# Kernel tuning notes

Measured on AMD Instinct MI355X. Metric: run time of the kernel, lower is better.

## Reference

```python
import jax, jax.numpy as jnp
import numpy as np

E = 16        # num_experts
H = 1024      # hidden_size
I = 768       # moe_intermediate_size
TOP_K = 2     # num_experts_per_tok
B, S = 1, 2048


def setup_inputs() -> dict:
    key = jax.random.key(0)
    ks = jax.random.split(key, 5)
    scale = 0.02
    return {
        "hidden_states": jax.random.normal(ks[0], (B, S, H), dtype=jnp.float32),
        "gate_w": jax.random.normal(ks[1], (E, H), dtype=jnp.float32) * scale,
        "gate_proj": jax.random.normal(ks[2], (E, I, H), dtype=jnp.float32) * scale,
        "up_proj": jax.random.normal(ks[3], (E, I, H), dtype=jnp.float32) * scale,
        "down_proj": jax.random.normal(ks[4], (E, H, I), dtype=jnp.float32) * scale,
    }


def reference(hidden_states, gate_w, gate_proj, up_proj, down_proj):
    b, s, h = hidden_states.shape
    x = hidden_states.reshape(-1, h)                        # [T, H]
    T = x.shape[0]

    # Router: logits -> fp32 softmax -> top-k -> renormalize (norm_topk_prob=True)
    router_logits = x @ gate_w.T                            # [T, E]
    probs = jax.nn.softmax(router_logits.astype(jnp.float32), axis=-1)
    top_vals, top_idx = jax.lax.top_k(probs, TOP_K)         # [T, k]
    top_vals = top_vals / jnp.sum(top_vals, axis=-1, keepdims=True)

    # Dense combine-weight matrix [T, E] (zero for unrouted experts)
    rw = jnp.zeros((T, E), dtype=jnp.float32)
    rw = rw.at[jnp.arange(T)[:, None], top_idx].add(top_vals)
    rw = rw.astype(hidden_states.dtype)

    # Expert SwiGLU MLPs (dense-over-experts reference for the grouped GEMM)
    g = jnp.einsum("th,eih->eti", x, gate_proj)             # [E, T, I]
    u = jnp.einsum("th,eih->eti", x, up_proj)               # [E, T, I]
    hmid = jax.nn.silu(g) * u                                # [E, T, I]
    expert_out = jnp.einsum("eti,ehi->eth", hmid, down_proj)  # [E, T, H]

    # Weighted combine
    out = jnp.einsum("eth,te->th", expert_out, rw)          # [T, H]
    return out.reshape(b, s, h)
```

## Files before the change

### kernel.cpp

```cpp
#include <hip/hip_runtime.h>
#include <hip/hip_bf16.h>
#include <cmath>

constexpr int T = 2048;
constexpr int H = 1024;
constexpr int I = 768;
constexpr int E = 16;
constexpr int WMAX = 48;

typedef short short8 __attribute__((ext_vector_type(8)));
typedef float f32x4  __attribute__((ext_vector_type(4)));

__device__ __forceinline__ short f2bf(float f) {
    __hip_bfloat16 h = __float2bfloat16(f);
    return *reinterpret_cast<short*>(&h);
}

__device__ __forceinline__ short8 pack8(float4 a, float4 b) {
    short8 v = {f2bf(a.x), f2bf(a.y), f2bf(a.z), f2bf(a.w),
                f2bf(b.x), f2bf(b.y), f2bf(b.z), f2bf(b.w)};
    return v;
}

__device__ __forceinline__ int sw(int r, int kg) {
    return r * 32 + (((kg + (r >> 1)) & 3) << 3);
}

__global__ __launch_bounds__(256) void cvt_x_kernel(
    const float* __restrict__ x, short* __restrict__ xb)
{
    size_t i = (size_t)blockIdx.x * 256 + threadIdx.x;
    const float4* s4 = (const float4*)x;
    float4 a = s4[2 * i], b = s4[2 * i + 1];
    *(short8*)(xb + i * 8) = pack8(a, b);
}

__global__ __launch_bounds__(256) void router_kernel(
    const float* __restrict__ x,
    const float* __restrict__ gw,
    int* __restrict__ cnt,
    int* __restrict__ entries,
    float* __restrict__ wlist)
{
    const int tid = threadIdx.x;
    const int tl = tid & 15, e = tid >> 4;
    const int t = blockIdx.x * 16 + tl;

    const float4* xr = (const float4*)(x + (size_t)t * H);
    const float4* gr = (const float4*)(gw + (size_t)e * H);
    float s0 = 0.f, s1 = 0.f;
    #pragma unroll 8
    for (int q = 0; q < 256; q += 2) {
        float4 a = xr[q],     b = gr[q];
        float4 c = xr[q + 1], d = gr[q + 1];
        s0 += a.x * b.x + a.y * b.y + a.z * b.z + a.w * b.w;
        s1 += c.x * d.x + c.y * d.y + c.z * d.z + c.w * d.w;
    }

    __shared__ float lg[16][17];
    lg[tl][e] = s0 + s1;
    __syncthreads();

    if (tid < 16) {
        int tk = blockIdx.x * 16 + tid;
        float v1 = -3.0e38f, v2 = -3.0e38f;
        int i1 = 0, i2 = 0;
        #pragma unroll
        for (int k = 0; k < E; ++k) {
            float v = lg[tid][k];
            if (v > v1) { v2 = v1; i2 = i1; v1 = v; i1 = k; }
            else if (v > v2) { v2 = v; i2 = k; }
        }
        float w1 = 1.f / (1.f + expf(v2 - v1));
        float w2 = 1.f - w1;
        int p = atomicAdd(&cnt[i1], 1);
        entries[i1 * T + p] = tk * 2;
        wlist[i1 * T + p] = w1;
        p = atomicAdd(&cnt[i2], 1);
        entries[i2 * T + p] = tk * 2 + 1;
        wlist[i2 * T + p] = w2;
    }
}

__global__ void build_worklist(const int* __restrict__ cnt,
                               int2* __restrict__ items,
                               int* __restrict__ nitems)
{
    if (threadIdx.x == 0) {
        int c = 0;
        for (int e = 0; e < E; ++e) {
            int n = cnt[e];
            for (int t0 = 0; t0 < n; t0 += 128) items[c++] = make_int2(e, t0);
        }
        *nitems = c;
    }
}

__global__ __launch_bounds__(256) void gateup_mfma(
    const short* __restrict__ xb,
    const float* __restrict__ gate_p,
    const float* __restrict__ up_p,
    const int* __restrict__ cnt,
    const int* __restrict__ entries,
    const int* __restrict__ nitems,
    const int2* __restrict__ items,
    short* __restrict__ hmid)
{
    if (blockIdx.x >= *nitems) return;
    const int e  = items[blockIdx.x].x;
    const int t0 = items[blockIdx.x].y;
    const int n  = cnt[e];
    const int i0 = blockIdx.y * 64;

    __shared__ short Xs[128 * 32];
    __shared__ short Gs[64 * 32];
    __shared__ short Us[64 * 32];
    __shared__ int toks[128];

    const int tid = threadIdx.x;
    if (tid < 128) {
        int r = t0 + tid;
        toks[tid] = (r < n) ? entries[e * T + r] : -1;
    }
    __syncthreads();

    const int lane = tid & 63, wave = tid >> 6;
    const int m16 = lane & 15, q = lane >> 4;

    const int sr = tid >> 2, skg = tid & 3;
    const int xt0 = toks[sr], xt1 = toks[64 + sr];
    const short* xsrc0 = xb + (size_t)((xt0 >= 0 ? xt0 : 0) >> 1) * H + skg * 8;
    const short* xsrc1 = xb + (size_t)((xt1 >= 0 ? xt1 : 0) >> 1) * H + skg * 8;
    const float* gsrc = gate_p + (size_t)e * I * H + (size_t)(i0 + sr) * H + skg * 8;
    const float* usrc = up_p   + (size_t)e * I * H + (size_t)(i0 + sr) * H + skg * 8;

    f32x4 accg[8], accu[8];
    #pragma unroll
    for (int a = 0; a < 8; ++a) {
        accg[a] = (f32x4){0.f, 0.f, 0.f, 0.f};
        accu[a] = (f32x4){0.f, 0.f, 0.f, 0.f};
    }

    short8 xc0 = *(const short8*)xsrc0;
    short8 xc1 = *(const short8*)xsrc1;
    float4 gc0 = *(const float4*)gsrc, gc1 = *(const float4*)(gsrc + 4);
    float4 uc0 = *(const float4*)usrc, uc1 = *(const float4*)(usrc + 4);

    for (int k0 = 0; k0 < H; k0 += 32) {
        *(short8*)&Xs[sw(sr, skg)]      = xc0;
        *(short8*)&Xs[sw(64 + sr, skg)] = xc1;
        *(short8*)&Gs[sw(sr, skg)] = pack8(gc0, gc1);
        *(short8*)&Us[sw(sr, skg)] = pack8(uc0, uc1);
        int kn = (k0 + 32 < H) ? k0 + 32 : 0;
        xc0 = *(const short8*)(xsrc0 + kn);
        xc1 = *(const short8*)(xsrc1 + kn);
        gc0 = *(const float4*)(gsrc + kn); gc1 = *(const float4*)(gsrc + kn + 4);
        uc0 = *(const float4*)(usrc + kn); uc1 = *(const float4*)(usrc + kn + 4);
        __syncthreads();

        short8 bg = *(const short8*)&Gs[sw(wave * 16 + m16, q)];
        short8 bu = *(const short8*)&Us[sw(wave * 16 + m16, q)];
        #pragma unroll
        for (int mi = 0; mi < 8; ++mi) {
            short8 af = *(const short8*)&Xs[sw(mi * 16 + m16, q)];
            accg[mi] = __builtin_amdgcn_mfma_f32_16x16x32_bf16(af, bg, accg[mi], 0, 0, 0);
            accu[mi] = __builtin_amdgcn_mfma_f32_16x16x32_bf16(af, bu, accu[mi], 0, 0, 0);
        }
        __syncthreads();
    }

    const int col = i0 + wave * 16 + m16;
    #pragma unroll
    for (int mi = 0; mi < 8; ++mi)
        #pragma unroll
        for (int j = 0; j < 4; ++j) {
            int row = mi * 16 + q * 4 + j;
            int slot = toks[row];
            if (slot < 0) continue;
            float g = accg[mi][j];
            float u = accu[mi][j];
            float hv = g / (1.f + expf(-g)) * u;
            ((unsigned short*)hmid)[(size_t)slot * I + col] = (unsigned short)f2bf(hv);
        }
}

__global__ __launch_bounds__(256) void down_mfma(
    const short* __restrict__ hmid,
    const float* __restrict__ down_p,
    const int* __restrict__ cnt,
    const int* __restrict__ entries,
    const float* __restrict__ wlist,
    const int* __restrict__ nitems,
    const int2* __restrict__ items,
    float* __restrict__ out)
{
    if (blockIdx.x >= *nitems) return;
    const int e  = items[blockIdx.x].x;
    const int t0 = items[blockIdx.x].y;
    const int n  = cnt[e];
    const int h0 = blockIdx.y * 128;

    __shared__ short As[128 * 32];
    __shared__ short Bs[128 * 32];
    __shared__ int toks[128];
    __shared__ float wr[128];

    const int tid = threadIdx.x;
    if (tid < 128) {
        int r = t0 + tid;
        bool v = (r < n);
        toks[tid] = v ? entries[e * T + r] : -1;
        wr[tid]   = v ? wlist[e * T + r] : 0.f;
    }
    __syncthreads();

    const int lane = tid & 63, wave = tid >> 6;
    const int m16 = lane & 15, q = lane >> 4;

    const int sr = tid >> 2, skg = tid & 3;
    const int at0 = toks[sr], at1 = toks[64 + sr];
    const short* asrc0 = hmid + (size_t)(at0 >= 0 ? at0 : 0) * I + skg * 8;
    const short* asrc1 = hmid + (size_t)(at1 >= 0 ? at1 : 0) * I + skg * 8;
    const float* bsrc0 = down_p + (size_t)e * H * I + (size_t)(h0 + sr) * I + skg * 8;
    const float* bsrc1 = down_p + (size_t)e * H * I + (size_t)(h0 + 64 + sr) * I + skg * 8;

    f32x4 acc[8][2];
    #pragma unroll
    for (int a = 0; a < 8; ++a)
        #pragma unroll
        for (int b = 0; b < 2; ++b)
            acc[a][b] = (f32x4){0.f, 0.f, 0.f, 0.f};

    short8 ac0 = *(const short8*)asrc0;
    short8 ac1 = *(const short8*)asrc1;
    float4 bc0 = *(const float4*)bsrc0, bc1 = *(const float4*)(bsrc0 + 4);
    float4 bc2 = *(const float4*)bsrc1, bc3 = *(const float4*)(bsrc1 + 4);

    for (int k0 = 0; k0 < I; k0 += 32) {
        *(short8*)&As[sw(sr, skg)]      = ac0;
        *(short8*)&As[sw(64 + sr, skg)] = ac1;
        *(short8*)&Bs[sw(sr, skg)]      = pack8(bc0, bc1);
        *(short8*)&Bs[sw(64 + sr, skg)] = pack8(bc2, bc3);
        int kn = (k0 + 32 < I) ? k0 + 32 : 0;
        ac0 = *(const short8*)(asrc0 + kn);
        ac1 = *(const short8*)(asrc1 + kn);
        bc0 = *(const float4*)(bsrc0 + kn); bc1 = *(const float4*)(bsrc0 + kn + 4);
        bc2 = *(const float4*)(bsrc1 + kn); bc3 = *(const float4*)(bsrc1 + kn + 4);
        __syncthreads();

        short8 bf0 = *(const short8*)&Bs[sw(wave * 32 + m16, q)];
        short8 bf1 = *(const short8*)&Bs[sw(wave * 32 + 16 + m16, q)];
        #pragma unroll
        for (int mi = 0; mi < 8; ++mi) {
            short8 af = *(const short8*)&As[sw(mi * 16 + m16, q)];
            acc[mi][0] = __builtin_amdgcn_mfma_f32_16x16x32_bf16(af, bf0, acc[mi][0], 0, 0, 0);
            acc[mi][1] = __builtin_amdgcn_mfma_f32_16x16x32_bf16(af, bf1, acc[mi][1], 0, 0, 0);
        }
        __syncthreads();
    }

    #pragma unroll
    for (int mi = 0; mi < 8; ++mi)
        #pragma unroll
        for (int ni = 0; ni < 2; ++ni)
            #pragma unroll
            for (int j = 0; j < 4; ++j) {
                int row = mi * 16 + q * 4 + j;
                int slot = toks[row];
                if (slot < 0) continue;
                int t = slot >> 1;
                float w = wr[row];
                int col = h0 + wave * 32 + ni * 16 + m16;
                atomicAdd(&out[(size_t)t * H + col], w * acc[mi][ni][j]);
            }
}

extern "C" void kernel_launch(void* const* d_in, const int* in_sizes, int n_in,
                              void* d_out, int out_size, void* d_ws, size_t ws_size,
                              hipStream_t stream) {
    const float* x  = (const float*)d_in[0];
    const float* gw = (const float*)d_in[1];
    const float* gp = (const float*)d_in[2];
    const float* up = (const float*)d_in[3];
    const float* dp = (const float*)d_in[4];
    float* out = (float*)d_out;

    char* ws = (char*)d_ws;
    int*   cnt     = (int*)ws;
    int*   nitems  = (int*)(ws + 64);
    int2*  items   = (int2*)(ws + 128);
    int*   entries = (int*)(ws + 2048);
    float* wlist   = (float*)(ws + 2048 + 131072);
    short* xb      = (short*)(ws + 2048 + 262144);
    short* hmid    = xb + (size_t)T * H;

    hipMemsetAsync(ws, 0, 2048, stream);
    hipMemsetAsync(out, 0, (size_t)T * H * sizeof(float), stream);

    cvt_x_kernel<<<T * H / 2048, 256, 0, stream>>>(x, xb);
    router_kernel<<<T / 16, 256, 0, stream>>>(x, gw, cnt, entries, wlist);
    build_worklist<<<1, 64, 0, stream>>>(cnt, items, nitems);
    gateup_mfma<<<dim3(WMAX, I / 64), 256, 0, stream>>>(
        xb, gp, up, cnt, entries, nitems, items, hmid);
    down_mfma<<<dim3(WMAX, H / 128), 256, 0, stream>>>(
        hmid, dp, cnt, entries, wlist, nitems, items, out);
}
```

Measured before the change: 307.4 us.

## Fuse x conversion into router, double-buffer LDS and shrink GEMM N-tiles

Folds the fp32-to-bf16 conversion of x into the router kernel, removing a separate launch. Both expert GEMM kernels get double-buffered shared memory, so the next K-slice is stored while MFMAs run on the current one, with one barrier per iteration instead of two. N-tiles shrink (64 to 32 columns for gate/up, 128 to 64 for down), doubling the grid for more parallelism, and each wave now owns a 32-row M slice. The cost is more blocks re-reading the same gathered activation rows and less reuse per weight tile.

New measurement: 317.7 us. 3.3% more time.

```diff
diff --git a/kernel.cpp b/kernel.cpp
--- a/kernel.cpp
+++ b/kernel.cpp
@@ -26,21 +26,13 @@
     return r * 32 + (((kg + (r >> 1)) & 3) << 3);
 }
 
-__global__ __launch_bounds__(256) void cvt_x_kernel(
-    const float* __restrict__ x, short* __restrict__ xb)
-{
-    size_t i = (size_t)blockIdx.x * 256 + threadIdx.x;
-    const float4* s4 = (const float4*)x;
-    float4 a = s4[2 * i], b = s4[2 * i + 1];
-    *(short8*)(xb + i * 8) = pack8(a, b);
-}
-
 __global__ __launch_bounds__(256) void router_kernel(
     const float* __restrict__ x,
     const float* __restrict__ gw,
     int* __restrict__ cnt,
     int* __restrict__ entries,
-    float* __restrict__ wlist)
+    float* __restrict__ wlist,
+    short* __restrict__ xb)
 {
     const int tid = threadIdx.x;
     const int tl = tid & 15, e = tid >> 4;
@@ -55,6 +47,15 @@
         float4 c = xr[q + 1], d = gr[q + 1];
         s0 += a.x * b.x + a.y * b.y + a.z * b.z + a.w * b.w;
         s1 += c.x * d.x + c.y * d.y + c.z * d.z + c.w * d.w;
+    }
+
+    {
+        const int row16 = tid >> 4, c16 = tid & 15;
+        const float4* src = (const float4*)(x + (size_t)(blockIdx.x * 16 + row16) * H + c16 * 64);
+        short* dst = xb + (size_t)(blockIdx.x * 16 + row16) * H + c16 * 64;
+        #pragma unroll
+        for (int j = 0; j < 8; ++j)
+            *(short8*)(dst + j * 8) = pack8(src[2 * j], src[2 * j + 1]);
     }
 
     __shared__ float lg[16][17];
@@ -110,11 +111,11 @@
     const int e  = items[blockIdx.x].x;
     const int t0 = items[blockIdx.x].y;
     const int n  = cnt[e];
-    const int i0 = blockIdx.y * 64;
-
-    __shared__ short Xs[128 * 32];
-    __shared__ short Gs[64 * 32];
-    __shared__ short Us[64 * 32];
+    const int i0 = blockIdx.y * 32;
+
+    __shared__ short Xs[2][128 * 32];
+    __shared__ short Gs[2][32 * 32];
+    __shared__ short Us[2][32 * 32];
     __shared__ int toks[128];
 
     const int tid = threadIdx.x;
@@ -126,62 +127,84 @@
 
     const int lane = tid & 63, wave = tid >> 6;
     const int m16 = lane & 15, q = lane >> 4;
+    const int wm = wave * 32;
 
     const int sr = tid >> 2, skg = tid & 3;
     const int xt0 = toks[sr], xt1 = toks[64 + sr];
     const short* xsrc0 = xb + (size_t)((xt0 >= 0 ? xt0 : 0) >> 1) * H + skg * 8;
     const short* xsrc1 = xb + (size_t)((xt1 >= 0 ? xt1 : 0) >> 1) * H + skg * 8;
-    const float* gsrc = gate_p + (size_t)e * I * H + (size_t)(i0 + sr) * H + skg * 8;
-    const float* usrc = up_p   + (size_t)e * I * H + (size_t)(i0 + sr) * H + skg * 8;
-
-    f32x4 accg[8], accu[8];
+    const int wt = tid >> 7;
+    const int st = tid & 127, wrr = st >> 2, wkg = st & 3;
+    const float* wsrc = (wt ? up_p : gate_p)
+        + (size_t)e * I * H + (size_t)(i0 + wrr) * H + wkg * 8;
+
+    f32x4 accg[2][2], accu[2][2];
     #pragma unroll
-    for (int a = 0; a < 8; ++a) {
-        accg[a] = (f32x4){0.f, 0.f, 0.f, 0.f};
-        accu[a] = (f32x4){0.f, 0.f, 0.f, 0.f};
-    }
-
-    short8 xc0 = *(const short8*)xsrc0;
-    short8 xc1 = *(const short8*)xsrc1;
-    float4 gc0 = *(const float4*)gsrc, gc1 = *(const float4*)(gsrc + 4);
-    float4 uc0 = *(const float4*)usrc, uc1 = *(const float4*)(usrc + 4);
-
-    for (int k0 = 0; k0 < H; k0 += 32) {
-        *(short8*)&Xs[sw(sr, skg)]      = xc0;
-        *(short8*)&Xs[sw(64 + sr, skg)] = xc1;
-        *(short8*)&Gs[sw(sr, skg)] = pack8(gc0, gc1);
-        *(short8*)&Us[sw(sr, skg)] = pack8(uc0, uc1);
-        int kn = (k0 + 32 < H) ? k0 + 32 : 0;
-        xc0 = *(const short8*)(xsrc0 + kn);
-        xc1 = *(const short8*)(xsrc1 + kn);
-        gc0 = *(const float4*)(gsrc + kn); gc1 = *(const float4*)(gsrc + kn + 4);
-        uc0 = *(const float4*)(usrc + kn); uc1 = *(const float4*)(usrc + kn + 4);
+    for (int a = 0; a < 2; ++a)
+        #pragma unroll
+        for (int b = 0; b < 2; ++b) {
+            accg[a][b] = (f32x4){0.f, 0.f, 0.f, 0.f};
+            accu[a][b] = (f32x4){0.f, 0.f, 0.f, 0.f};
+        }
+
+    {
+        short8 x0 = *(const short8*)xsrc0;
+        short8 x1 = *(const short8*)xsrc1;
+        float4 wa = *(const float4*)wsrc, wb = *(const float4*)(wsrc + 4);
+        *(short8*)&Xs[0][sw(sr, skg)]      = x0;
+        *(short8*)&Xs[0][sw(64 + sr, skg)] = x1;
+        short8 pw = pack8(wa, wb);
+        if (wt == 0) *(short8*)&Gs[0][sw(wrr, wkg)] = pw;
+        else         *(short8*)&Us[0][sw(wrr, wkg)] = pw;
+    }
+    __syncthreads();
+
+    constexpr int NIT = H / 32;
+    for (int it = 0; it < NIT; ++it) {
+        const int cur = it & 1, nxt = cur ^ 1;
+        const int kn = (it + 1 < NIT) ? (it + 1) * 32 : 0;
+        short8 nx0 = *(const short8*)(xsrc0 + kn);
+        short8 nx1 = *(const short8*)(xsrc1 + kn);
+        float4 nwa = *(const float4*)(wsrc + kn), nwb = *(const float4*)(wsrc + kn + 4);
+
+        short8 af0 = *(const short8*)&Xs[cur][sw(wm + m16, q)];
+        short8 af1 = *(const short8*)&Xs[cur][sw(wm + 16 + m16, q)];
+        short8 bg0 = *(const short8*)&Gs[cur][sw(m16, q)];
+        short8 bg1 = *(const short8*)&Gs[cur][sw(16 + m16, q)];
+        short8 bu0 = *(const short8*)&Us[cur][sw(m16, q)];
+        short8 bu1 = *(const short8*)&Us[cur][sw(16 + m16, q)];
+        accg[0][0] = __builtin_amdgcn_mfma_f32_16x16x32_bf16(af0, bg0, accg[0][0], 0, 0, 0);
+        accg[1][0] = __builtin_amdgcn_mfma_f32_16x16x32_bf16(af1, bg0, accg[1][0], 0, 0, 0);
+        accg[0][1] = __builtin_amdgcn_mfma_f32_16x16x32_bf16(af0, bg1, accg[0][1], 0, 0, 0);
+        accg[1][1] = __builtin_amdgcn_mfma_f32_16x16x32_bf16(af1, bg1, accg[1][1], 0, 0, 0);
+        accu[0][0] = __builtin_amdgcn_mfma_f32_16x16x32_bf16(af0, bu0, accu[0][0], 0, 0, 0);
+        accu[1][0] = __builtin_amdgcn_mfma_f32_16x16x32_bf16(af1, bu0, accu[1][0], 0, 0, 0);
+        accu[0][1] = __builtin_amdgcn_mfma_f32_16x16x32_bf16(af0, bu1, accu[0][1], 0, 0, 0);
+        accu[1][1] = __builtin_amdgcn_mfma_f32_16x16x32_bf16(af1, bu1, accu[1][1], 0, 0, 0);
+
+        *(short8*)&Xs[nxt][sw(sr, skg)]      = nx0;
+        *(short8*)&Xs[nxt][sw(64 + sr, skg)] = nx1;
+        short8 pw = pack8(nwa, nwb);
+        if (wt == 0) *(short8*)&Gs[nxt][sw(wrr, wkg)] = pw;
+        else         *(short8*)&Us[nxt][sw(wrr, wkg)] = pw;
         __syncthreads();
-
-        short8 bg = *(const short8*)&Gs[sw(wave * 16 + m16, q)];
-        short8 bu = *(const short8*)&Us[sw(wave * 16 + m16, q)];
-        #pragma unroll
-        for (int mi = 0; mi < 8; ++mi) {
-            short8 af = *(const short8*)&Xs[sw(mi * 16 + m16, q)];
-            accg[mi] = __builtin_amdgcn_mfma_f32_16x16x32_bf16(af, bg, accg[mi], 0, 0, 0);
-            accu[mi] = __builtin_amdgcn_mfma_f32_16x16x32_bf16(af, bu, accu[mi], 0, 0, 0);
-        }
-        __syncthreads();
-    }
-
-    const int col = i0 + wave * 16 + m16;
+    }
+
     #pragma unroll
-    for (int mi = 0; mi < 8; ++mi)
-        #pragma unroll
-        for (int j = 0; j < 4; ++j) {
-            int row = mi * 16 + q * 4 + j;
-            int slot = toks[row];
-            if (slot < 0) continue;
-            float g = accg[mi][j];
-            float u = accu[mi][j];
-            float hv = g / (1.f + expf(-g)) * u;
-            ((unsigned short*)hmid)[(size_t)slot * I + col] = (unsigned short)f2bf(hv);
-        }
+    for (int mi = 0; mi < 2; ++mi)
+        #pragma unroll
+        for (int ni = 0; ni < 2; ++ni)
+            #pragma unroll
+            for (int j = 0; j < 4; ++j) {
+                int row = wm + mi * 16 + q * 4 + j;
+                int slot = toks[row];
+                if (slot < 0) continue;
+                float g = accg[mi][ni][j];
+                float u = accu[mi][ni][j];
+                float hv = g / (1.f + expf(-g)) * u;
+                int col = i0 + ni * 16 + m16;
+                ((unsigned short*)hmid)[(size_t)slot * I + col] = (unsigned short)f2bf(hv);
+            }
 }
 
 __global__ __launch_bounds__(256) void down_mfma(
@@ -198,10 +221,10 @@
     const int e  = items[blockIdx.x].x;
     const int t0 = items[blockIdx.x].y;
     const int n  = cnt[e];
-    const int h0 = blockIdx.y * 128;
-
-    __shared__ short As[128 * 32];
-    __shared__ short Bs[128 * 32];
+    const int h0 = blockIdx.y * 64;
+
+    __shared__ short As[2][128 * 32];
+    __shared__ short Bs[2][64 * 32];
     __shared__ int toks[128];
     __shared__ float wr[128];
 
@@ -216,61 +239,66 @@
 
     const int lane = tid & 63, wave = tid >> 6;
     const int m16 = lane & 15, q = lane >> 4;
+    const int wm = wave * 32;
 
     const int sr = tid >> 2, skg = tid & 3;
     const int at0 = toks[sr], at1 = toks[64 + sr];
     const short* asrc0 = hmid + (size_t)(at0 >= 0 ? at0 : 0) * I + skg * 8;
     const short* asrc1 = hmid + (size_t)(at1 >= 0 ? at1 : 0) * I + skg * 8;
-    const float* bsrc0 = down_p + (size_t)e * H * I + (size_t)(h0 + sr) * I + skg * 8;
-    const float* bsrc1 = down_p + (size_t)e * H * I + (size_t)(h0 + 64 + sr) * I + skg * 8;
-
-    f32x4 acc[8][2];
+    const float* bsrc = down_p + (size_t)e * H * I + (size_t)(h0 + sr) * I + skg * 8;
+
+    f32x4 acc[2][4];
     #pragma unroll
-    for (int a = 0; a < 8; ++a)
-        #pragma unroll
-        for (int b = 0; b < 2; ++b)
+    for (int a = 0; a < 2; ++a)
+        #pragma unroll
+        for (int b = 0; b < 4; ++b)
             acc[a][b] = (f32x4){0.f, 0.f, 0.f, 0.f};
 
-    short8 ac0 = *(const short8*)asrc0;
-    short8 ac1 = *(const short8*)asrc1;
-    float4 bc0 = *(const float4*)bsrc0, bc1 = *(const float4*)(bsrc0 + 4);
-    float4 bc2 = *(const float4*)bsrc1, bc3 = *(const float4*)(bsrc1 + 4);
-
-    for (int k0 = 0; k0 < I; k0 += 32) {
-        *(short8*)&As[sw(sr, skg)]      = ac0;
-        *(short8*)&As[sw(64 + sr, skg)] = ac1;
-        *(short8*)&Bs[sw(sr, skg)]      = pack8(bc0, bc1);
-        *(short8*)&Bs[sw(64 + sr, skg)] = pack8(bc2, bc3);
-        int kn = (k0 + 32 < I) ? k0 + 32 : 0;
-        ac0 = *(const short8*)(asrc0 + kn);
-        ac1 = *(const short8*)(asrc1 + kn);
-        bc0 = *(const float4*)(bsrc0 + kn); bc1 = *(const float4*)(bsrc0 + kn + 4);
-        bc2 = *(const float4*)(bsrc1 + kn); bc3 = *(const float4*)(bsrc1 + kn + 4);
+    {
+        short8 a0 = *(const short8*)asrc0;
+        short8 a1 = *(const short8*)asrc1;
+        float4 ba = *(const float4*)bsrc, bb = *(const float4*)(bsrc + 4);
+        *(short8*)&As[0][sw(sr, skg)]      = a0;
+        *(short8*)&As[0][sw(64 + sr, skg)] = a1;
+        *(short8*)&Bs[0][sw(sr, skg)] = pack8(ba, bb);
+    }
+    __syncthreads();
+
+    constexpr int NIT = I / 32;
+    for (int it = 0; it < NIT; ++it) {
+        const int cur = it & 1, nxt = cur ^ 1;
+        const int kn = (it + 1 < NIT) ? (it + 1) * 32 : 0;
+        short8 na0 = *(const short8*)(asrc0 + kn);
+        short8 na1 = *(const short8*)(asrc1 + kn);
+        float4 nba = *(const float4*)(bsrc + kn), nbb = *(const float4*)(bsrc + kn + 4);
+
+        short8 af0 = *(const short8*)&As[cur][sw(wm + m16, q)];
+        short8 af1 = *(const short8*)&As[cur][sw(wm + 16 + m16, q)];
+        #pragma unroll
+        for (int ni = 0; ni < 4; ++ni) {
+            short8 bfr = *(const short8*)&Bs[cur][sw(ni * 16 + m16, q)];
+            acc[0][ni] = __builtin_amdgcn_mfma_f32_16x16x32_bf16(af0, bfr, acc[0][ni], 0, 0, 0);
+            acc[1][ni] = __builtin_amdgcn_mfma_f32_16x16x32_bf16(af1, bfr, acc[1][ni], 0, 0, 0);
+        }
+
+        *(short8*)&As[nxt][sw(sr, skg)]      = na0;
+        *(short8*)&As[nxt][sw(64 + sr, skg)] = na1;
+        *(short8*)&Bs[nxt][sw(sr, skg)] = pack8(nba, nbb);
         __syncthreads();
-
-        short8 bf0 = *(const short8*)&Bs[sw(wave * 32 + m16, q)];
-        short8 bf1 = *(const short8*)&Bs[sw(wave * 32 + 16 + m16, q)];
-        #pragma unroll
-        for (int mi = 0; mi < 8; ++mi) {
-            short8 af = *(const short8*)&As[sw(mi * 16 + m16, q)];
-            acc[mi][0] = __builtin_amdgcn_mfma_f32_16x16x32_bf16(af, bf0, acc[mi][0], 0, 0, 0);
-            acc[mi][1] = __builtin_amdgcn_mfma_f32_16x16x32_bf16(af, bf1, acc[mi][1], 0, 0, 0);
-        }
-        __syncthreads();
     }
 
     #pragma unroll
-    for (int mi = 0; mi < 8; ++mi)
-        #pragma unroll
-        for (int ni = 0; ni < 2; ++ni)
+    for (int mi = 0; mi < 2; ++mi)
+        #pragma unroll
+        for (int ni = 0; ni < 4; ++ni)
             #pragma unroll
             for (int j = 0; j < 4; ++j) {
-                int row = mi * 16 + q * 4 + j;
+                int row = wm + mi * 16 + q * 4 + j;
                 int slot = toks[row];
                 if (slot < 0) continue;
                 int t = slot >> 1;
                 float w = wr[row];
-                int col = h0 + wave * 32 + ni * 16 + m16;
+                int col = h0 + ni * 16 + m16;
                 atomicAdd(&out[(size_t)t * H + col], w * acc[mi][ni][j]);
             }
 }
@@ -297,11 +325,10 @@
     hipMemsetAsync(ws, 0, 2048, stream);
     hipMemsetAsync(out, 0, (size_t)T * H * sizeof(float), stream);
 
-    cvt_x_kernel<<<T * H / 2048, 256, 0, stream>>>(x, xb);
-    router_kernel<<<T / 16, 256, 0, stream>>>(x, gw, cnt, entries, wlist);
+    router_kernel<<<T / 16, 256, 0, stream>>>(x, gw, cnt, entries, wlist, xb);
     build_worklist<<<1, 64, 0, stream>>>(cnt, items, nitems);
-    gateup_mfma<<<dim3(WMAX, I / 64), 256, 0, stream>>>(
+    gateup_mfma<<<dim3(WMAX, I / 32), 256, 0, stream>>>(
         xb, gp, up, cnt, entries, nitems, items, hmid);
-    down_mfma<<<dim3(WMAX, H / 128), 256, 0, stream>>>(
+    down_mfma<<<dim3(WMAX, H / 64), 256, 0, stream>>>(
         hmid, dp, cnt, entries, wlist, nitems, items, out);
 }
```
